# Optimization experiments

Measured on AMD Instinct MI355X. Metric: run time of the kernel, lower is better.

Reference implementation:

```python
import jax, jax.numpy as jnp
import numpy as np

D_MODEL = 1024
NUM_HEADS = 16
HEAD_DIM = D_MODEL // NUM_HEADS


def setup_inputs() -> dict:
    key = jax.random.key(0)
    ks = jax.random.split(key, 5)
    B, S = 2, 2048
    x = jax.random.normal(ks[0], (B, S, D_MODEL), dtype=jnp.float32)
    Wq = jax.random.normal(ks[1], (D_MODEL, D_MODEL), dtype=jnp.float32) * 0.02
    Wk = jax.random.normal(ks[2], (D_MODEL, D_MODEL), dtype=jnp.float32) * 0.02
    Wv = jax.random.normal(ks[3], (D_MODEL, D_MODEL), dtype=jnp.float32) * 0.02
    Wo = jax.random.normal(ks[4], (D_MODEL, D_MODEL), dtype=jnp.float32) * 0.02
    return {"x": x, "Wq": Wq, "Wk": Wk, "Wv": Wv, "Wo": Wo}


def reference(x, Wq, Wk, Wv, Wo):
    B, S, _ = x.shape
    # QKV projections (Linear is x @ W, no bias)
    q = (x @ Wq).reshape(B, S, NUM_HEADS, HEAD_DIM).transpose(0, 2, 1, 3)  # [B,H,S,Dh]
    k = (x @ Wk).reshape(B, S, NUM_HEADS, HEAD_DIM).transpose(0, 2, 1, 3)
    v = (x @ Wv).reshape(B, S, NUM_HEADS, HEAD_DIM).transpose(0, 2, 1, 3)
    scale = 1.0 / jnp.sqrt(jnp.asarray(HEAD_DIM, dtype=x.dtype))
    scores = jnp.einsum("bhqd,bhkd->bhqk", q, k) * scale  # [B,H,S,S]
    causal = jnp.tril(jnp.ones((S, S), dtype=bool))
    scores = jnp.where(causal, scores, -jnp.inf)
    probs = jax.nn.softmax(scores, axis=-1)
    out = jnp.einsum("bhqk,bhkd->bhqd", probs, v)  # [B,H,S,Dh]
    out = out.transpose(0, 2, 1, 3).reshape(B, S, D_MODEL)
    return out @ Wo
```

## Files before the change

### kernel.cpp

```cpp
#include <hip/hip_runtime.h>

typedef __attribute__((ext_vector_type(4))) short short4v;
typedef __attribute__((ext_vector_type(8))) short short8v;
typedef __attribute__((ext_vector_type(4))) float float4v;
typedef __attribute__((ext_vector_type(4))) int int4v;

#define GLD_LDS16(gsrc, ldst)                                                             \
    __builtin_amdgcn_global_load_lds(                                                     \
        (const __attribute__((address_space(1))) void*)(gsrc),                            \
        (__attribute__((address_space(3))) void*)(ldst), 16, 0, 0)

__device__ __forceinline__ short f2bf(float f) {
    unsigned u = __builtin_bit_cast(unsigned, f);
    u += 0x7fffu + ((u >> 16) & 1u);
    return (short)(u >> 16);
}

__global__ void k_cvt_x(const float* __restrict__ x, short* __restrict__ xb) {
    int i = blockIdx.x * blockDim.x + threadIdx.x;
    float4v v = ((const float4v*)x)[i];
    short4v o;
    o[0] = f2bf(v[0]); o[1] = f2bf(v[1]); o[2] = f2bf(v[2]); o[3] = f2bf(v[3]);
    ((short4v*)xb)[i] = o;
}

__global__ void k_transpose(const float* __restrict__ W0, const float* __restrict__ W1,
                            const float* __restrict__ W2, const float* __restrict__ W3,
                            short* __restrict__ Wt) {
    const float* W = blockIdx.z == 0 ? W0 : blockIdx.z == 1 ? W1 : blockIdx.z == 2 ? W2 : W3;
    short* dst = Wt + (size_t)blockIdx.z * 1024 * 1024;
    __shared__ float tile[32][33];
    int x0 = blockIdx.x * 32, y0 = blockIdx.y * 32;
    int tx = threadIdx.x, ty = threadIdx.y;
#pragma unroll
    for (int j = 0; j < 4; j++) {
        int r = ty + j * 8;
        tile[r][tx] = W[(size_t)(y0 + r) * 1024 + x0 + tx];
    }
    __syncthreads();
#pragma unroll
    for (int j = 0; j < 4; j++) {
        int r = ty + j * 8;
        dst[(size_t)(x0 + r) * 1024 + y0 + tx] = f2bf(tile[tx][r]);
    }
}

template <int MODE>
__launch_bounds__(512, 4)
__global__ void k_gemm2(const short* __restrict__ A, const short* __restrict__ Bt,
                        short* __restrict__ out0, short* __restrict__ out1,
                        float* __restrict__ outF) {
    __shared__ short As[2][128][64];
    __shared__ short Bs[2][128][64];
    int t = threadIdx.x;
    int l = t & 63, w = t >> 6;
    int wm = w >> 2, wn = w & 3;
    int lr = l & 15, lg = l >> 4;
    int m0 = blockIdx.x * 128, n0 = blockIdx.y * 128;
    const short* Bp = Bt + (MODE == 0 ? ((size_t)blockIdx.z << 20) : 0);

    int srow = l >> 3;
    int sg = (l & 7) ^ srow;
    const short* Ab0 = A + (size_t)(m0 + w * 8 + srow) * 1024 + sg * 8;
    const short* Ab1 = Ab0 + 64 * 1024;
    const short* Bb0 = Bp + (size_t)(n0 + w * 8 + srow) * 1024 + sg * 8;
    const short* Bb1 = Bb0 + 64 * 1024;

    float4v acc[4][2] = {};

#define STAGE(bb, k0)                                   \
    do {                                                \
        GLD_LDS16(Ab0 + (k0), &As[bb][w * 8][0]);       \
        GLD_LDS16(Ab1 + (k0), &As[bb][64 + w * 8][0]);  \
        GLD_LDS16(Bb0 + (k0), &Bs[bb][w * 8][0]);       \
        GLD_LDS16(Bb1 + (k0), &Bs[bb][64 + w * 8][0]);  \
    } while (0)

    STAGE(0, 0);
    __syncthreads();
    int cur = 0;

    for (int kt = 0; kt < 16; kt++) {
        if (kt + 1 < 16) STAGE(cur ^ 1, (kt + 1) * 64);
#pragma unroll
        for (int ks = 0; ks < 2; ks++) {
            short8v af[4], bfv[2];
            int hh = ks * 4 + lg;
            int sw = ((hh ^ (lr & 7)) * 8);
#pragma unroll
            for (int fm = 0; fm < 4; fm++)
                af[fm] = *(const short8v*)&As[cur][wm * 64 + fm * 16 + lr][sw];
#pragma unroll
            for (int fn = 0; fn < 2; fn++)
                bfv[fn] = *(const short8v*)&Bs[cur][wn * 32 + fn * 16 + lr][sw];
            __builtin_amdgcn_s_setprio(1);
#pragma unroll
            for (int fm = 0; fm < 4; fm++)
#pragma unroll
                for (int fn = 0; fn < 2; fn++)
                    acc[fm][fn] = (MODE == 1)
                        ? __builtin_amdgcn_mfma_f32_16x16x32_bf16(bfv[fn], af[fm], acc[fm][fn], 0, 0, 0)
                        : __builtin_amdgcn_mfma_f32_16x16x32_bf16(af[fm], bfv[fn], acc[fm][fn], 0, 0, 0);
            __builtin_amdgcn_s_setprio(0);
        }
        __syncthreads();
        cur ^= 1;
    }
#undef STAGE

    if (MODE == 0) {
        short* out = (blockIdx.z == 0) ? out0 : out1;
        float scale = (blockIdx.z == 0) ? 0.125f * 1.44269504088896f : 1.0f;
#pragma unroll
        for (int fm = 0; fm < 4; fm++)
#pragma unroll
            for (int fn = 0; fn < 2; fn++)
#pragma unroll
                for (int r = 0; r < 4; r++) {
                    int m = m0 + wm * 64 + fm * 16 + lg * 4 + r;
                    int n = n0 + wn * 32 + fn * 16 + lr;
                    float v = acc[fm][fn][r] * scale;
                    int b = m >> 11, s = m & 2047, h = n >> 6, dh = n & 63;
                    out[(((size_t)(b * 16 + h)) * 2048 + s) * 64 + dh] = f2bf(v);
                }
    } else if (MODE == 1) {
#pragma unroll
        for (int fm = 0; fm < 4; fm++)
#pragma unroll
            for (int fn = 0; fn < 2; fn++)
#pragma unroll
                for (int r = 0; r < 4; r++) {
                    int n = n0 + wn * 32 + fn * 16 + lg * 4 + r;
                    int m = m0 + wm * 64 + fm * 16 + lr;
                    int b = m >> 11, s = m & 2047, h = n >> 6, dh = n & 63;
                    out0[(((size_t)(b * 16 + h)) * 64 + dh) * 2048 + s] = f2bf(acc[fm][fn][r]);
                }
    } else {
#pragma unroll
        for (int fm = 0; fm < 4; fm++)
#pragma unroll
            for (int fn = 0; fn < 2; fn++)
#pragma unroll
                for (int r = 0; r < 4; r++) {
                    int m = m0 + wm * 64 + fm * 16 + lg * 4 + r;
                    int n = n0 + wn * 32 + fn * 16 + lr;
                    outF[(size_t)m * 1024 + n] = acc[fm][fn][r];
                }
    }
}

__launch_bounds__(256, 2)
__global__ void k_attn(const short* __restrict__ Qb, const short* __restrict__ Kb,
                       const short* __restrict__ Vtb, short* __restrict__ Ob) {
    __shared__ short K_lds[2][64][64];
    __shared__ short V_lds[2][64][64];
    __shared__ short p_lds[4][2][16][64];
    int t = threadIdx.x;
    int l = t & 63, w = t >> 6;
    int lr = l & 15, lg = l >> 4;

    int L = blockIdx.x;
    int bh, tile;
    if (L < 256) { bh = L & 31; tile = 15 - (L >> 5); }
    else         { int j = L - 256; bh = j & 31; tile = j >> 5; }
    int nch = 2 * tile + 2;

    const short* Qp = Qb + (size_t)bh * 2048 * 64;
    const short* Kp = Kb + (size_t)bh * 2048 * 64;
    const short* Vp = Vtb + (size_t)bh * 64 * 2048;

    auto stage = [&](int bb, int kv0) {
#pragma unroll
        for (int i = 0; i < 2; i++) {
            int s = t + i * 256;
            int row = s >> 3, cg = s & 7;
            int cs = (cg ^ (row & 7)) * 8;
            GLD_LDS16(&Kp[(size_t)(kv0 + row) * 64 + cs], (short*)K_lds[bb] + (size_t)s * 8);
            GLD_LDS16(&Vp[(size_t)row * 2048 + kv0 + cs], (short*)V_lds[bb] + (size_t)s * 8);
        }
    };

    stage(0, 0);

    int q0a = tile * 128 + w * 32;
    int q0b = q0a + 16;
    short8v qf0a = *(const short8v*)&Qp[(size_t)(q0a + lr) * 64 + lg * 8];
    short8v qf1a = *(const short8v*)&Qp[(size_t)(q0a + lr) * 64 + 32 + lg * 8];
    short8v qf0b = *(const short8v*)&Qp[(size_t)(q0b + lr) * 64 + lg * 8];
    short8v qf1b = *(const short8v*)&Qp[(size_t)(q0b + lr) * 64 + 32 + lg * 8];

    float4v oa[4] = {}, ob[4] = {};
    float mra[4] = {-3e38f, -3e38f, -3e38f, -3e38f};
    float mrb[4] = {-3e38f, -3e38f, -3e38f, -3e38f};
    float lsa[4] = {0.f, 0.f, 0.f, 0.f};
    float lsb[4] = {0.f, 0.f, 0.f, 0.f};
    int cur = 0;
    int b = bh >> 4, h = bh & 15;

    auto softmax_store = [&](float4v (&s)[4], float (&mr)[4], float (&ls)[4],
                             float4v (&o)[4], int X) {
        float mx[4];
#pragma unroll
        for (int r = 0; r < 4; r++)
            mx[r] = fmaxf(fmaxf(s[0][r], s[1][r]), fmaxf(s[2][r], s[3][r]));
        float worst = fmaxf(fmaxf(mx[0] - mr[0], mx[1] - mr[1]),
                            fmaxf(mx[2] - mr[2], mx[3] - mr[3]));
        if (!__all(worst <= 8.f)) {
#pragma unroll
            for (int r = 0; r < 4; r++) {
                float m_ = mx[r];
                m_ = fmaxf(m_, __shfl_xor(m_, 1));
                m_ = fmaxf(m_, __shfl_xor(m_, 2));
                m_ = fmaxf(m_, __shfl_xor(m_, 4));
                m_ = fmaxf(m_, __shfl_xor(m_, 8));
                float mnew = fmaxf(mr[r], m_);
                float sc = __builtin_amdgcn_exp2f(mr[r] - mnew);
                mr[r] = mnew;
                ls[r] *= sc;
                o[0][r] *= sc; o[1][r] *= sc; o[2][r] *= sc; o[3][r] *= sc;
            }
        }
        int bg = lr >> 3, co = lr & 7;
#pragma unroll
        for (int r = 0; r < 4; r++) {
            int row = 4 * lg + r, rx = row & 7;
            float e0 = __builtin_amdgcn_exp2f(s[0][r] - mr[r]);
            float e1 = __builtin_amdgcn_exp2f(s[1][r] - mr[r]);
            float e2 = __builtin_amdgcn_exp2f(s[2][r] - mr[r]);
            float e3 = __builtin_amdgcn_exp2f(s[3][r] - mr[r]);
            ls[r] += (e0 + e1) + (e2 + e3);
            p_lds[w][X][row][((bg    ) ^ rx) * 8 + co] = f2bf(e0);
            p_lds[w][X][row][((bg + 2) ^ rx) * 8 + co] = f2bf(e1);
            p_lds[w][X][row][((bg + 4) ^ rx) * 8 + co] = f2bf(e2);
            p_lds[w][X][row][((bg + 6) ^ rx) * 8 + co] = f2bf(e3);
        }
    };

    __syncthreads();

    for (int ci = 0; ci < nch; ci++) {
        int kv0 = ci * 64;

        if (ci + 1 < nch) stage(cur ^ 1, (ci + 1) * 64);

        const short* Kf = (const short*)K_lds[cur];
        float4v sa[4] = {}, sb[4] = {};
        __builtin_amdgcn_s_setprio(1);
#pragma unroll
        for (int t4 = 0; t4 < 4; t4++) {
            int krow = t4 * 16 + lr;
            int sw = (krow & 7);
            short8v kfa = *(const short8v*)&Kf[krow * 64 + ((lg ^ sw) * 8)];
            short8v kfb = *(const short8v*)&Kf[krow * 64 + (((lg ^ 4) ^ sw) * 8)];
            sa[t4] = __builtin_amdgcn_mfma_f32_16x16x32_bf16(qf0a, kfa, sa[t4], 0, 0, 0);
            sa[t4] = __builtin_amdgcn_mfma_f32_16x16x32_bf16(qf1a, kfb, sa[t4], 0, 0, 0);
            sb[t4] = __builtin_amdgcn_mfma_f32_16x16x32_bf16(qf0b, kfa, sb[t4], 0, 0, 0);
            sb[t4] = __builtin_amdgcn_mfma_f32_16x16x32_bf16(qf1b, kfb, sb[t4], 0, 0, 0);
        }
        __builtin_amdgcn_s_setprio(0);

        if (kv0 + 63 > q0a) {
#pragma unroll
            for (int t4 = 0; t4 < 4; t4++)
#pragma unroll
                for (int r = 0; r < 4; r++)
                    if (kv0 + t4 * 16 + lr > q0a + lg * 4 + r) sa[t4][r] = -3e38f;
        }
        if (kv0 + 63 > q0b) {
#pragma unroll
            for (int t4 = 0; t4 < 4; t4++)
#pragma unroll
                for (int r = 0; r < 4; r++)
                    if (kv0 + t4 * 16 + lr > q0b + lg * 4 + r) sb[t4][r] = -3e38f;
        }

        softmax_store(sa, mra, lsa, oa, 0);
        softmax_store(sb, mrb, lsb, ob, 1);

        int prx = lr & 7;
        short8v pa0 = *(const short8v*)&p_lds[w][0][lr][8 * (lg ^ prx)];
        short8v pa1 = *(const short8v*)&p_lds[w][0][lr][8 * ((4 + lg) ^ prx)];
        short8v pb0 = *(const short8v*)&p_lds[w][1][lr][8 * (lg ^ prx)];
        short8v pb1 = *(const short8v*)&p_lds[w][1][lr][8 * ((4 + lg) ^ prx)];

        const short* Vf = (const short*)V_lds[cur];
        __builtin_amdgcn_s_setprio(1);
#pragma unroll
        for (int dt = 0; dt < 4; dt++) {
            int vrow = dt * 16 + lr;
            int sw = (vrow & 7);
            short8v vfa = *(const short8v*)&Vf[vrow * 64 + ((lg ^ sw) * 8)];
            short8v vfb = *(const short8v*)&Vf[vrow * 64 + (((lg ^ 4) ^ sw) * 8)];
            oa[dt] = __builtin_amdgcn_mfma_f32_16x16x32_bf16(pa0, vfa, oa[dt], 0, 0, 0);
            oa[dt] = __builtin_amdgcn_mfma_f32_16x16x32_bf16(pa1, vfb, oa[dt], 0, 0, 0);
            ob[dt] = __builtin_amdgcn_mfma_f32_16x16x32_bf16(pb0, vfa, ob[dt], 0, 0, 0);
            ob[dt] = __builtin_amdgcn_mfma_f32_16x16x32_bf16(pb1, vfb, ob[dt], 0, 0, 0);
        }
        __builtin_amdgcn_s_setprio(0);

        __syncthreads();
        cur ^= 1;
    }

    float inva[4], invb[4];
#pragma unroll
    for (int r = 0; r < 4; r++) {
        float va = lsa[r], vb = lsb[r];
        va += __shfl_xor(va, 1); va += __shfl_xor(va, 2);
        va += __shfl_xor(va, 4); va += __shfl_xor(va, 8);
        vb += __shfl_xor(vb, 1); vb += __shfl_xor(vb, 2);
        vb += __shfl_xor(vb, 4); vb += __shfl_xor(vb, 8);
        inva[r] = 1.0f / va;
        invb[r] = 1.0f / vb;
    }
#pragma unroll
    for (int dt = 0; dt < 4; dt++)
#pragma unroll
        for (int r = 0; r < 4; r++) {
            int qa = q0a + lg * 4 + r;
            int qb = q0b + lg * 4 + r;
            Ob[((size_t)(b * 2048 + qa)) * 1024 + h * 64 + dt * 16 + lr] = f2bf(oa[dt][r] * inva[r]);
            Ob[((size_t)(b * 2048 + qb)) * 1024 + h * 64 + dt * 16 + lr] = f2bf(ob[dt][r] * invb[r]);
        }
}

extern "C" void kernel_launch(void* const* d_in, const int* in_sizes, int n_in,
                              void* d_out, int out_size, void* d_ws, size_t ws_size,
                              hipStream_t stream) {
    const float* x  = (const float*)d_in[0];
    const float* Wq = (const float*)d_in[1];
    const float* Wk = (const float*)d_in[2];
    const float* Wv = (const float*)d_in[3];
    const float* Wo = (const float*)d_in[4];
    float* out = (float*)d_out;

    char* ws = (char*)d_ws;
    short* xb  = (short*)(ws);
    short* Wtb = (short*)(ws + 8388608);
    short* Qb  = (short*)(ws + 16777216);
    short* Kb  = (short*)(ws + 25165824);
    short* Vtb = (short*)(ws + 33554432);
    short* Ob  = (short*)(ws + 41943040);

    k_cvt_x<<<4096, 256, 0, stream>>>(x, xb);
    k_transpose<<<dim3(32, 32, 4), dim3(32, 8), 0, stream>>>(Wq, Wk, Wv, Wo, Wtb);
    k_gemm2<0><<<dim3(32, 8, 2), 512, 0, stream>>>(xb, Wtb, Qb, Kb, nullptr);
    k_gemm2<1><<<dim3(32, 8), 512, 0, stream>>>(xb, Wtb + 2 * 1048576, Vtb, nullptr, nullptr);
    k_attn<<<512, 256, 0, stream>>>(Qb, Kb, Vtb, Ob);
    k_gemm2<2><<<dim3(32, 8), 512, 0, stream>>>(Ob, Wtb + 3 * 1048576, nullptr, nullptr, out);
}
```

Before: 121.8 us.

## Merge Q/K/V projections into one launch and shrink attention tiles to 64 rows

Combines the Q/K projection launch and the V projection launch into a single 3-slice grid, so the V GEMM no longer runs as a separate small launch. The attention kernel moves from 256-thread blocks over 128 query rows to 128-thread blocks over 64 query rows, giving 1024 blocks with heavy-first causal ordering. The aim is to cut launch overhead and improve load balance and occupancy for the causal attention. In exchange, each K/V chunk staged in LDS is reused by fewer query rows, which raises global traffic per block.

```diff
diff --git a/kernel.cpp b/kernel.cpp
--- a/kernel.cpp
+++ b/kernel.cpp
@@ -45,10 +45,126 @@
     }
 }
 
-template <int MODE>
 __launch_bounds__(512, 4)
-__global__ void k_gemm2(const short* __restrict__ A, const short* __restrict__ Bt,
-                        short* __restrict__ out0, short* __restrict__ out1,
+__global__ void k_gemmQKV(const short* __restrict__ A, const short* __restrict__ Wtb,
+                          short* __restrict__ Qb, short* __restrict__ Kb,
+                          short* __restrict__ Vtb) {
+    __shared__ short As[2][128][64];
+    __shared__ short Bs[2][128][64];
+    int t = threadIdx.x;
+    int l = t & 63, w = t >> 6;
+    int wm = w >> 2, wn = w & 3;
+    int lr = l & 15, lg = l >> 4;
+    int m0 = blockIdx.x * 128, n0 = blockIdx.y * 128;
+    int which = blockIdx.z;
+    const short* Bp = Wtb + ((size_t)which << 20);
+
+    int srow = l >> 3;
+    int sg = (l & 7) ^ srow;
+    const short* Ab0 = A + (size_t)(m0 + w * 8 + srow) * 1024 + sg * 8;
+    const short* Ab1 = Ab0 + 64 * 1024;
+    const short* Bb0 = Bp + (size_t)(n0 + w * 8 + srow) * 1024 + sg * 8;
+    const short* Bb1 = Bb0 + 64 * 1024;
+
+    float4v acc[4][2] = {};
+
+#define STAGE(bb, k0)                                   \
+    do {                                                \
+        GLD_LDS16(Ab0 + (k0), &As[bb][w * 8][0]);       \
+        GLD_LDS16(Ab1 + (k0), &As[bb][64 + w * 8][0]);  \
+        GLD_LDS16(Bb0 + (k0), &Bs[bb][w * 8][0]);       \
+        GLD_LDS16(Bb1 + (k0), &Bs[bb][64 + w * 8][0]);  \
+    } while (0)
+
+    STAGE(0, 0);
+    __syncthreads();
+    int cur = 0;
+
+    if (which == 2) {
+        for (int kt = 0; kt < 16; kt++) {
+            if (kt + 1 < 16) STAGE(cur ^ 1, (kt + 1) * 64);
+#pragma unroll
+            for (int ks = 0; ks < 2; ks++) {
+                short8v af[4], bfv[2];
+                int hh = ks * 4 + lg;
+                int sw = ((hh ^ (lr & 7)) * 8);
+#pragma unroll
+                for (int fm = 0; fm < 4; fm++)
+                    af[fm] = *(const short8v*)&As[cur][wm * 64 + fm * 16 + lr][sw];
+#pragma unroll
+                for (int fn = 0; fn < 2; fn++)
+                    bfv[fn] = *(const short8v*)&Bs[cur][wn * 32 + fn * 16 + lr][sw];
+                __builtin_amdgcn_s_setprio(1);
+#pragma unroll
+                for (int fm = 0; fm < 4; fm++)
+#pragma unroll
+                    for (int fn = 0; fn < 2; fn++)
+                        acc[fm][fn] = __builtin_amdgcn_mfma_f32_16x16x32_bf16(bfv[fn], af[fm], acc[fm][fn], 0, 0, 0);
+                __builtin_amdgcn_s_setprio(0);
+            }
+            __syncthreads();
+            cur ^= 1;
+        }
+    } else {
+        for (int kt = 0; kt < 16; kt++) {
+            if (kt + 1 < 16) STAGE(cur ^ 1, (kt + 1) * 64);
+#pragma unroll
+            for (int ks = 0; ks < 2; ks++) {
+                short8v af[4], bfv[2];
+                int hh = ks * 4 + lg;
+                int sw = ((hh ^ (lr & 7)) * 8);
+#pragma unroll
+                for (int fm = 0; fm < 4; fm++)
+                    af[fm] = *(const short8v*)&As[cur][wm * 64 + fm * 16 + lr][sw];
+#pragma unroll
+                for (int fn = 0; fn < 2; fn++)
+                    bfv[fn] = *(const short8v*)&Bs[cur][wn * 32 + fn * 16 + lr][sw];
+                __builtin_amdgcn_s_setprio(1);
+#pragma unroll
+                for (int fm = 0; fm < 4; fm++)
+#pragma unroll
+                    for (int fn = 0; fn < 2; fn++)
+                        acc[fm][fn] = __builtin_amdgcn_mfma_f32_16x16x32_bf16(af[fm], bfv[fn], acc[fm][fn], 0, 0, 0);
+                __builtin_amdgcn_s_setprio(0);
+            }
+            __syncthreads();
+            cur ^= 1;
+        }
+    }
+#undef STAGE
+
+    if (which < 2) {
+        short* out = (which == 0) ? Qb : Kb;
+        float scale = (which == 0) ? 0.125f * 1.44269504088896f : 1.0f;
+#pragma unroll
+        for (int fm = 0; fm < 4; fm++)
+#pragma unroll
+            for (int fn = 0; fn < 2; fn++)
+#pragma unroll
+                for (int r = 0; r < 4; r++) {
+                    int m = m0 + wm * 64 + fm * 16 + lg * 4 + r;
+                    int n = n0 + wn * 32 + fn * 16 + lr;
+                    float v = acc[fm][fn][r] * scale;
+                    int b = m >> 11, s = m & 2047, h = n >> 6, dh = n & 63;
+                    out[(((size_t)(b * 16 + h)) * 2048 + s) * 64 + dh] = f2bf(v);
+                }
+    } else {
+#pragma unroll
+        for (int fm = 0; fm < 4; fm++)
+#pragma unroll
+            for (int fn = 0; fn < 2; fn++)
+#pragma unroll
+                for (int r = 0; r < 4; r++) {
+                    int n = n0 + wn * 32 + fn * 16 + lg * 4 + r;
+                    int m = m0 + wm * 64 + fm * 16 + lr;
+                    int b = m >> 11, s = m & 2047, h = n >> 6, dh = n & 63;
+                    Vtb[(((size_t)(b * 16 + h)) * 64 + dh) * 2048 + s] = f2bf(acc[fm][fn][r]);
+                }
+    }
+}
+
+__launch_bounds__(512, 4)
+__global__ void k_gemmO(const short* __restrict__ A, const short* __restrict__ Bt,
                         float* __restrict__ outF) {
     __shared__ short As[2][128][64];
     __shared__ short Bs[2][128][64];
@@ -57,13 +173,12 @@
     int wm = w >> 2, wn = w & 3;
     int lr = l & 15, lg = l >> 4;
     int m0 = blockIdx.x * 128, n0 = blockIdx.y * 128;
-    const short* Bp = Bt + (MODE == 0 ? ((size_t)blockIdx.z << 20) : 0);
 
     int srow = l >> 3;
     int sg = (l & 7) ^ srow;
     const short* Ab0 = A + (size_t)(m0 + w * 8 + srow) * 1024 + sg * 8;
     const short* Ab1 = Ab0 + 64 * 1024;
-    const short* Bb0 = Bp + (size_t)(n0 + w * 8 + srow) * 1024 + sg * 8;
+    const short* Bb0 = Bt + (size_t)(n0 + w * 8 + srow) * 1024 + sg * 8;
     const short* Bb1 = Bb0 + 64 * 1024;
 
     float4v acc[4][2] = {};
@@ -98,9 +213,7 @@
             for (int fm = 0; fm < 4; fm++)
 #pragma unroll
                 for (int fn = 0; fn < 2; fn++)
-                    acc[fm][fn] = (MODE == 1)
-                        ? __builtin_amdgcn_mfma_f32_16x16x32_bf16(bfv[fn], af[fm], acc[fm][fn], 0, 0, 0)
-                        : __builtin_amdgcn_mfma_f32_16x16x32_bf16(af[fm], bfv[fn], acc[fm][fn], 0, 0, 0);
+                    acc[fm][fn] = __builtin_amdgcn_mfma_f32_16x16x32_bf16(af[fm], bfv[fn], acc[fm][fn], 0, 0, 0);
             __builtin_amdgcn_s_setprio(0);
         }
         __syncthreads();
@@ -108,62 +221,33 @@
     }
 #undef STAGE
 
-    if (MODE == 0) {
-        short* out = (blockIdx.z == 0) ? out0 : out1;
-        float scale = (blockIdx.z == 0) ? 0.125f * 1.44269504088896f : 1.0f;
-#pragma unroll
-        for (int fm = 0; fm < 4; fm++)
-#pragma unroll
-            for (int fn = 0; fn < 2; fn++)
-#pragma unroll
-                for (int r = 0; r < 4; r++) {
-                    int m = m0 + wm * 64 + fm * 16 + lg * 4 + r;
-                    int n = n0 + wn * 32 + fn * 16 + lr;
-                    float v = acc[fm][fn][r] * scale;
-                    int b = m >> 11, s = m & 2047, h = n >> 6, dh = n & 63;
-                    out[(((size_t)(b * 16 + h)) * 2048 + s) * 64 + dh] = f2bf(v);
-                }
-    } else if (MODE == 1) {
-#pragma unroll
-        for (int fm = 0; fm < 4; fm++)
-#pragma unroll
-            for (int fn = 0; fn < 2; fn++)
-#pragma unroll
-                for (int r = 0; r < 4; r++) {
-                    int n = n0 + wn * 32 + fn * 16 + lg * 4 + r;
-                    int m = m0 + wm * 64 + fm * 16 + lr;
-                    int b = m >> 11, s = m & 2047, h = n >> 6, dh = n & 63;
-                    out0[(((size_t)(b * 16 + h)) * 64 + dh) * 2048 + s] = f2bf(acc[fm][fn][r]);
-                }
-    } else {
-#pragma unroll
-        for (int fm = 0; fm < 4; fm++)
-#pragma unroll
-            for (int fn = 0; fn < 2; fn++)
-#pragma unroll
-                for (int r = 0; r < 4; r++) {
-                    int m = m0 + wm * 64 + fm * 16 + lg * 4 + r;
-                    int n = n0 + wn * 32 + fn * 16 + lr;
-                    outF[(size_t)m * 1024 + n] = acc[fm][fn][r];
-                }
-    }
-}
-
-__launch_bounds__(256, 2)
+#pragma unroll
+    for (int fm = 0; fm < 4; fm++)
+#pragma unroll
+        for (int fn = 0; fn < 2; fn++)
+#pragma unroll
+            for (int r = 0; r < 4; r++) {
+                int m = m0 + wm * 64 + fm * 16 + lg * 4 + r;
+                int n = n0 + wn * 32 + fn * 16 + lr;
+                outF[(size_t)m * 1024 + n] = acc[fm][fn][r];
+            }
+}
+
+__launch_bounds__(128, 4)
 __global__ void k_attn(const short* __restrict__ Qb, const short* __restrict__ Kb,
                        const short* __restrict__ Vtb, short* __restrict__ Ob) {
     __shared__ short K_lds[2][64][64];
     __shared__ short V_lds[2][64][64];
-    __shared__ short p_lds[4][2][16][64];
+    __shared__ short p_lds[2][2][16][64];
     int t = threadIdx.x;
     int l = t & 63, w = t >> 6;
     int lr = l & 15, lg = l >> 4;
 
     int L = blockIdx.x;
-    int bh, tile;
-    if (L < 256) { bh = L & 31; tile = 15 - (L >> 5); }
-    else         { int j = L - 256; bh = j & 31; tile = j >> 5; }
-    int nch = 2 * tile + 2;
+    int bh = L & 31;
+    int g = (L >> 5) & 15;
+    int tile = (L < 512) ? (31 - g) : g;
+    int nch = tile + 1;
 
     const short* Qp = Qb + (size_t)bh * 2048 * 64;
     const short* Kp = Kb + (size_t)bh * 2048 * 64;
@@ -171,8 +255,8 @@
 
     auto stage = [&](int bb, int kv0) {
 #pragma unroll
-        for (int i = 0; i < 2; i++) {
-            int s = t + i * 256;
+        for (int i = 0; i < 4; i++) {
+            int s = t + i * 128;
             int row = s >> 3, cg = s & 7;
             int cs = (cg ^ (row & 7)) * 8;
             GLD_LDS16(&Kp[(size_t)(kv0 + row) * 64 + cs], (short*)K_lds[bb] + (size_t)s * 8);
@@ -182,7 +266,7 @@
 
     stage(0, 0);
 
-    int q0a = tile * 128 + w * 32;
+    int q0a = tile * 64 + w * 32;
     int q0b = q0a + 16;
     short8v qf0a = *(const short8v*)&Qp[(size_t)(q0a + lr) * 64 + lg * 8];
     short8v qf1a = *(const short8v*)&Qp[(size_t)(q0a + lr) * 64 + 32 + lg * 8];
@@ -344,8 +428,7 @@
 
     k_cvt_x<<<4096, 256, 0, stream>>>(x, xb);
     k_transpose<<<dim3(32, 32, 4), dim3(32, 8), 0, stream>>>(Wq, Wk, Wv, Wo, Wtb);
-    k_gemm2<0><<<dim3(32, 8, 2), 512, 0, stream>>>(xb, Wtb, Qb, Kb, nullptr);
-    k_gemm2<1><<<dim3(32, 8), 512, 0, stream>>>(xb, Wtb + 2 * 1048576, Vtb, nullptr, nullptr);
-    k_attn<<<512, 256, 0, stream>>>(Qb, Kb, Vtb, Ob);
-    k_gemm2<2><<<dim3(32, 8), 512, 0, stream>>>(Ob, Wtb + 3 * 1048576, nullptr, nullptr, out);
-}
+    k_gemmQKV<<<dim3(32, 8, 3), 512, 0, stream>>>(xb, Wtb, Qb, Kb, Vtb);
+    k_attn<<<1024, 128, 0, stream>>>(Qb, Kb, Vtb, Ob);
+    k_gemmO<<<dim3(32, 8), 512, 0, stream>>>(Ob, Wtb + 3 * 1048576, out);
+}
```

New measurement: 127.4 us. 1.05x slower.
